# Kernel tuning notes

Measured on AMD Instinct MI355X. Metric: run time of the kernel, lower is better.

The kernel has to match this reference:

```python
import jax, jax.numpy as jnp
import numpy as np

HIDDEN = 2048
INTER = 768
N_EXPERTS = 16
TOP_K = 2
B, S = 4, 2048


def setup_inputs() -> dict:
    key = jax.random.key(0)
    ks = jax.random.split(key, 5)
    scale = 0.02
    return {
        "hidden_states": jax.random.normal(ks[0], (B, S, HIDDEN), dtype=jnp.float32),
        # nn.Linear weight layout: [out_features, in_features]
        "gate_w": jax.random.normal(ks[1], (N_EXPERTS, HIDDEN), dtype=jnp.float32) * scale,
        "w_gate": jax.random.normal(ks[2], (N_EXPERTS, INTER, HIDDEN), dtype=jnp.float32) * scale,
        "w_up": jax.random.normal(ks[3], (N_EXPERTS, INTER, HIDDEN), dtype=jnp.float32) * scale,
        "w_down": jax.random.normal(ks[4], (N_EXPERTS, HIDDEN, INTER), dtype=jnp.float32) * scale,
    }


def _moe_forward(hidden_states, gate_w, w_gate, w_up, w_down):
    b, s, h = hidden_states.shape
    x = hidden_states.reshape(-1, h)                      # [T, H]
    t = x.shape[0]
    logits = x @ gate_w.T                                 # [T, E]
    probs = jax.nn.softmax(logits, axis=-1)
    top_vals, top_idx = jax.lax.top_k(probs, TOP_K)       # [T, K]
    top_vals = top_vals / jnp.sum(top_vals, axis=-1, keepdims=True)
    # combine weights per token per expert (zero if not routed)
    comb = jnp.zeros((t, N_EXPERTS), dtype=x.dtype)
    comb = comb.at[jnp.arange(t)[:, None], top_idx].add(top_vals)  # [T, E]

    out = jnp.zeros_like(x)
    for e in range(N_EXPERTS):  # small fixed loop over experts
        g = x @ w_gate[e].T                               # [T, I]
        u = x @ w_up[e].T                                 # [T, I]
        y = (jax.nn.silu(g) * u) @ w_down[e].T            # [T, H]
        out = out + comb[:, e:e + 1] * y
    return out.reshape(b, s, h)


def reference(hidden_states, gate_w, w_gate, w_up, w_down):
    return _moe_forward(hidden_states, gate_w, w_gate, w_up, w_down)
```

## Files before the change

### kernel.cpp

```cpp
#include <hip/hip_runtime.h>
#include <hip/hip_bf16.h>

#define NTOK 8192
#define HID 2048
#define INTER 768
#define NEXP 16

typedef __bf16 bf16x8 __attribute__((ext_vector_type(8)));
typedef float f32x4 __attribute__((ext_vector_type(4)));

typedef const __attribute__((address_space(1))) void gvoid_t;
typedef __attribute__((address_space(3))) void lvoid_t;

static __device__ __forceinline__ void load_lds16(const void* g, void* l) {
  __builtin_amdgcn_global_load_lds((gvoid_t*)g, (lvoid_t*)l, 16, 0, 0);
}

static __device__ __forceinline__ unsigned short f2bf(float f) {
  unsigned int u = __float_as_uint(f);
  u += 0x7FFFu + ((u >> 16) & 1u);
  return (unsigned short)(u >> 16);
}

static __device__ __forceinline__ float bf2f(unsigned short b) {
  return __uint_as_float(((unsigned int)b) << 16);
}

#define SYNC_PIPE                                     \
  asm volatile("s_waitcnt vmcnt(0)" ::: "memory");    \
  __builtin_amdgcn_s_barrier();

__global__ __launch_bounds__(256) void cvt3_kernel(
    const float* __restrict__ s0, const float* __restrict__ s1, const float* __restrict__ s2,
    unsigned short* __restrict__ dst0, unsigned short* __restrict__ dst1,
    unsigned short* __restrict__ dst2, int n) {
  const float* src = (blockIdx.y == 0) ? s0 : (blockIdx.y == 1) ? s1 : s2;
  unsigned short* dst = (blockIdx.y == 0) ? dst0 : (blockIdx.y == 1) ? dst1 : dst2;
  int i = (blockIdx.x * 256 + threadIdx.x) * 4;
  int stride = gridDim.x * 256 * 4;
  for (; i < n; i += stride) {
    float4 v = *reinterpret_cast<const float4*>(src + i);
    ushort4 o;
    o.x = f2bf(v.x); o.y = f2bf(v.y); o.z = f2bf(v.z); o.w = f2bf(v.w);
    *reinterpret_cast<ushort4*>(dst + i) = o;
  }
}

__global__ __launch_bounds__(256) void router_kernel(const float* __restrict__ x,
                                                     const float* __restrict__ gw,
                                                     int* __restrict__ te,
                                                     float* __restrict__ tw,
                                                     unsigned short* __restrict__ Xb) {
  const int lane = threadIdx.x & 63;
  const int wid = threadIdx.x >> 6;
  const int t0 = (blockIdx.x * 4 + wid) * 2;
  const float4* xa = reinterpret_cast<const float4*>(x + (size_t)t0 * HID);
  const float4* xb = xa + HID / 4;
  const float4* g4 = reinterpret_cast<const float4*>(gw);

  float4 va[8], vb[8];
#pragma unroll
  for (int j = 0; j < 8; ++j) {
    va[j] = xa[lane + 64 * j];
    vb[j] = xb[lane + 64 * j];
  }
  ushort4* oa = reinterpret_cast<ushort4*>(Xb + (size_t)t0 * HID);
  ushort4* ob = oa + HID / 4;
#pragma unroll
  for (int j = 0; j < 8; ++j) {
    ushort4 u;
    u.x = f2bf(va[j].x); u.y = f2bf(va[j].y); u.z = f2bf(va[j].z); u.w = f2bf(va[j].w);
    oa[lane + 64 * j] = u;
    u.x = f2bf(vb[j].x); u.y = f2bf(vb[j].y); u.z = f2bf(vb[j].z); u.w = f2bf(vb[j].w);
    ob[lane + 64 * j] = u;
  }

  float accA[NEXP], accB[NEXP];
#pragma unroll
  for (int e = 0; e < NEXP; ++e) { accA[e] = 0.f; accB[e] = 0.f; }
#pragma unroll
  for (int e = 0; e < NEXP; ++e) {
#pragma unroll
    for (int j = 0; j < 8; ++j) {
      float4 g = g4[e * (HID / 4) + lane + 64 * j];
      accA[e] += va[j].x * g.x + va[j].y * g.y + va[j].z * g.z + va[j].w * g.w;
      accB[e] += vb[j].x * g.x + vb[j].y * g.y + vb[j].z * g.z + vb[j].w * g.w;
    }
  }
#pragma unroll
  for (int e = 0; e < NEXP; ++e) {
#pragma unroll
    for (int m = 32; m >= 1; m >>= 1) {
      accA[e] += __shfl_xor(accA[e], m);
      accB[e] += __shfl_xor(accB[e], m);
    }
  }
  if (lane == 0) {
#pragma unroll
    for (int k = 0; k < 2; ++k) {
      const float* acc = k ? accB : accA;
      int t = t0 + k;
      float b0 = -1e30f; int i0 = 0;
#pragma unroll
      for (int e = 0; e < NEXP; ++e) { if (acc[e] > b0) { b0 = acc[e]; i0 = e; } }
      float b1 = -1e30f; int i1 = 0;
#pragma unroll
      for (int e = 0; e < NEXP; ++e) { if (e != i0 && acc[e] > b1) { b1 = acc[e]; i1 = e; } }
      float w0 = 1.f / (1.f + __expf(b1 - b0));
      te[2 * t] = i0; te[2 * t + 1] = i1;
      tw[2 * t] = w0; tw[2 * t + 1] = 1.f - w0;
    }
  }
}

__global__ __launch_bounds__(256) void build_kernel(
    const int* __restrict__ te, const float* __restrict__ tw,
    int* __restrict__ counts, int* __restrict__ offsets,
    int* __restrict__ tok_flat, float* __restrict__ w_flat,
    int* __restrict__ tok_slot,
    int* __restrict__ tile_map, int* __restrict__ n_tiles) {
  __shared__ int lds_cnt[NEXP][257];
  __shared__ int lds_off[NEXP];
  const int tid = threadIdx.x;
  const int lane = tid & 63;
  const int wv = tid >> 6;

  int cnt[NEXP];
#pragma unroll
  for (int ex = 0; ex < NEXP; ++ex) cnt[ex] = 0;
  for (int i = 0; i < 64; ++i) {
    int e = te[tid * 64 + i];
#pragma unroll
    for (int ex = 0; ex < NEXP; ++ex) cnt[ex] += (e == ex) ? 1 : 0;
  }
#pragma unroll
  for (int ex = 0; ex < NEXP; ++ex) lds_cnt[ex][tid] = cnt[ex];
  __syncthreads();

  for (int ex = wv * 4; ex < wv * 4 + 4; ++ex) {
    int carry = 0;
    for (int c = 0; c < 4; ++c) {
      int v = lds_cnt[ex][c * 64 + lane];
      int s = v;
#pragma unroll
      for (int d = 1; d < 64; d <<= 1) {
        int o = __shfl_up(s, d);
        if (lane >= d) s += o;
      }
      lds_cnt[ex][c * 64 + lane] = carry + s - v;
      carry += __shfl(s, 63);
    }
    if (lane == 0) lds_cnt[ex][256] = carry;
  }
  __syncthreads();

  if (tid == 0) {
    int run = 0, nt = 0;
    for (int e = 0; e < NEXP; ++e) {
      int tot = lds_cnt[e][256];
      counts[e] = tot;
      offsets[e] = run;
      lds_off[e] = run;
      for (int m0 = 0; m0 < tot; m0 += 128) tile_map[nt++] = (e << 16) | m0;
      run += tot;
    }
    *n_tiles = nt;
  }
  __syncthreads();

  int base[NEXP];
#pragma unroll
  for (int ex = 0; ex < NEXP; ++ex) base[ex] = lds_off[ex] + lds_cnt[ex][tid];
  for (int i = 0; i < 64; ++i) {
    int idx = tid * 64 + i;
    int e = te[idx];
    float w = tw[idx];
    int pos = 0;
#pragma unroll
    for (int ex = 0; ex < NEXP; ++ex) {
      if (e == ex) { pos = base[ex]; base[ex] = pos + 1; }
    }
    tok_flat[pos] = idx >> 1;
    w_flat[pos] = w;
    tok_slot[idx] = pos;
  }
}

__global__ __launch_bounds__(256, 2) void gemm_gu_kernel(
    const unsigned short* __restrict__ Xb,
    const unsigned short* __restrict__ Wg,
    const unsigned short* __restrict__ Wu,
    const int* __restrict__ counts, const int* __restrict__ offsets,
    const int* __restrict__ tok_flat,
    const int* __restrict__ tile_map, const int* __restrict__ n_tiles,
    unsigned short* __restrict__ Hf) {
  const int bid = blockIdx.x;
  const int cpx = gridDim.x >> 3;
  const int wg = (bid & 7) * cpx + (bid >> 3);
  const int y = wg / 6;
  if (y >= *n_tiles) return;
  const int xb = wg - y * 6;
  const int tm = tile_map[y];
  const int e = tm >> 16, m0 = tm & 0xFFFF;
  const int cnt = counts[e];
  const int off = offsets[e];
  const int n0 = xb * 128;

  __shared__ __align__(16) unsigned short As0[128 * 32], As1[128 * 32];
  __shared__ __align__(16) unsigned short Bg0[128 * 32], Bg1[128 * 32];
  __shared__ __align__(16) unsigned short Bu0[128 * 32], Bu1[128 * 32];

  const int tid = threadIdx.x;
  const int lane = tid & 63;
  const int wid = tid >> 6;
  const int rl = tid >> 2;
  const int srcc = ((tid & 3) ^ ((tid >> 3) & 3)) * 8;
  const int d0 = tid * 8;
  const int d1 = d0 + 64 * 32;

  const int r0 = m0 + rl, r1 = r0 + 64;
  const int s0 = (r0 < cnt) ? off + r0 : off;
  const int s1 = (r1 < cnt) ? off + r1 : off;
  const unsigned short* aptr0 = Xb + (size_t)tok_flat[s0] * HID + srcc;
  const unsigned short* aptr1 = Xb + (size_t)tok_flat[s1] * HID + srcc;
  const unsigned short* gptr0 = Wg + ((size_t)e * INTER + n0 + rl) * HID + srcc;
  const unsigned short* gptr1 = gptr0 + (size_t)64 * HID;
  const unsigned short* uptr0 = Wu + ((size_t)e * INTER + n0 + rl) * HID + srcc;
  const unsigned short* uptr1 = uptr0 + (size_t)64 * HID;

  f32x4 zero = {0.f, 0.f, 0.f, 0.f};
  f32x4 accG[4][4], accU[4][4];
#pragma unroll
  for (int i = 0; i < 4; ++i)
#pragma unroll
    for (int j = 0; j < 4; ++j) { accG[i][j] = zero; accU[i][j] = zero; }

  const int wm = (wid >> 1) * 64;
  const int wn = (wid & 1) * 64;
  const int fr = lane & 15;
  const int cs = (((lane >> 4) ^ ((lane >> 1) & 3)) * 8);

#define STAGE_GU(AS, BGS, BUS, kt)           \
  {                                          \
    load_lds16(aptr0 + (kt), (AS) + d0);     \
    load_lds16(aptr1 + (kt), (AS) + d1);     \
    load_lds16(gptr0 + (kt), (BGS) + d0);    \
    load_lds16(gptr1 + (kt), (BGS) + d1);    \
    load_lds16(uptr0 + (kt), (BUS) + d0);    \
    load_lds16(uptr1 + (kt), (BUS) + d1);    \
  }

#define COMPUTE_GU(AS, BGS, BUS)                                                       \
  {                                                                                    \
    bf16x8 af[4], bg[4], bu[4];                                                        \
    _Pragma("unroll") for (int i = 0; i < 4; ++i) {                                    \
      af[i] = *reinterpret_cast<const bf16x8*>((AS) + (wm + i * 16 + fr) * 32 + cs);   \
      bg[i] = *reinterpret_cast<const bf16x8*>((BGS) + (wn + i * 16 + fr) * 32 + cs);  \
      bu[i] = *reinterpret_cast<const bf16x8*>((BUS) + (wn + i * 16 + fr) * 32 + cs);  \
    }                                                                                  \
    _Pragma("unroll") for (int i = 0; i < 4; ++i)                                      \
      _Pragma("unroll") for (int j = 0; j < 4; ++j) {                                  \
        accG[i][j] = __builtin_amdgcn_mfma_f32_16x16x32_bf16(af[i], bg[j], accG[i][j], 0, 0, 0); \
        accU[i][j] = __builtin_amdgcn_mfma_f32_16x16x32_bf16(af[i], bu[j], accU[i][j], 0, 0, 0); \
      }                                                                                \
  }

  STAGE_GU(As0, Bg0, Bu0, 0);
  SYNC_PIPE
#pragma unroll 1
  for (int kt = 0; kt < HID; kt += 64) {
    STAGE_GU(As1, Bg1, Bu1, kt + 32);
    COMPUTE_GU(As0, Bg0, Bu0);
    SYNC_PIPE
    if (kt + 64 < HID) STAGE_GU(As0, Bg0, Bu0, kt + 64);
    COMPUTE_GU(As1, Bg1, Bu1);
    SYNC_PIPE
  }
#undef STAGE_GU
#undef COMPUTE_GU

  const int lr = (lane >> 4) * 4;
  const int lc = lane & 15;
#pragma unroll
  for (int i = 0; i < 4; ++i) {
#pragma unroll
    for (int r = 0; r < 4; ++r) {
      int m = wm + i * 16 + lr + r;
      if (m0 + m < cnt) {
        size_t base = (size_t)(off + m0 + m) * INTER + (size_t)(n0 + wn + lc);
#pragma unroll
        for (int j = 0; j < 4; ++j) {
          float g = accG[i][j][r];
          float u = accU[i][j][r];
          float h = g / (1.f + __expf(-g)) * u;
          Hf[base + j * 16] = f2bf(h);
        }
      }
    }
  }
}

__global__ __launch_bounds__(256, 3) void gemm_y_kernel(
    const unsigned short* __restrict__ Hf,
    const unsigned short* __restrict__ Wd,
    const int* __restrict__ counts, const int* __restrict__ offsets,
    const float* __restrict__ w_flat,
    const int* __restrict__ tile_map, const int* __restrict__ n_tiles,
    unsigned short* __restrict__ Yf) {
  const int bid = blockIdx.x;
  const int cpx = gridDim.x >> 3;
  const int wg = (bid & 7) * cpx + (bid >> 3);
  const int y = wg / 16;
  if (y >= *n_tiles) return;
  const int xb = wg - y * 16;
  const int tm = tile_map[y];
  const int e = tm >> 16, m0 = tm & 0xFFFF;
  const int cnt = counts[e];
  const int off = offsets[e];
  const int n0 = xb * 128;

  __shared__ __align__(16) unsigned short As0[128 * 32], As1[128 * 32];
  __shared__ __align__(16) unsigned short Bs0[128 * 32], Bs1[128 * 32];

  const int tid = threadIdx.x;
  const int lane = tid & 63;
  const int wid = tid >> 6;
  const int rl = tid >> 2;
  const int srcc = ((tid & 3) ^ ((tid >> 3) & 3)) * 8;
  const int d0 = tid * 8;
  const int d1 = d0 + 64 * 32;

  const int r0 = m0 + rl, r1 = r0 + 64;
  const int s0 = (r0 < cnt) ? off + r0 : off;
  const int s1 = (r1 < cnt) ? off + r1 : off;
  const unsigned short* aptr0 = Hf + (size_t)s0 * INTER + srcc;
  const unsigned short* aptr1 = Hf + (size_t)s1 * INTER + srcc;
  const unsigned short* bptr0 = Wd + ((size_t)e * HID + n0 + rl) * INTER + srcc;
  const unsigned short* bptr1 = bptr0 + (size_t)64 * INTER;

  f32x4 zero = {0.f, 0.f, 0.f, 0.f};
  f32x4 acc[4][4];
#pragma unroll
  for (int i = 0; i < 4; ++i)
#pragma unroll
    for (int j = 0; j < 4; ++j) acc[i][j] = zero;

  const int wm = (wid >> 1) * 64;
  const int wn = (wid & 1) * 64;
  const int fr = lane & 15;
  const int cs = (((lane >> 4) ^ ((lane >> 1) & 3)) * 8);

#define STAGE_Y(AS, BS, kt)               \
  {                                       \
    load_lds16(aptr0 + (kt), (AS) + d0);  \
    load_lds16(aptr1 + (kt), (AS) + d1);  \
    load_lds16(bptr0 + (kt), (BS) + d0);  \
    load_lds16(bptr1 + (kt), (BS) + d1);  \
  }

#define COMPUTE_Y(AS, BS)                                                              \
  {                                                                                    \
    bf16x8 af[4], bf_[4];                                                              \
    _Pragma("unroll") for (int i = 0; i < 4; ++i) {                                    \
      af[i] = *reinterpret_cast<const bf16x8*>((AS) + (wm + i * 16 + fr) * 32 + cs);   \
      bf_[i] = *reinterpret_cast<const bf16x8*>((BS) + (wn + i * 16 + fr) * 32 + cs);  \
    }                                                                                  \
    _Pragma("unroll") for (int i = 0; i < 4; ++i)                                      \
      _Pragma("unroll") for (int j = 0; j < 4; ++j)                                    \
        acc[i][j] = __builtin_amdgcn_mfma_f32_16x16x32_bf16(af[i], bf_[j], acc[i][j], 0, 0, 0); \
  }

  STAGE_Y(As0, Bs0, 0);
  SYNC_PIPE
#pragma unroll 1
  for (int kt = 0; kt < INTER; kt += 64) {
    STAGE_Y(As1, Bs1, kt + 32);
    COMPUTE_Y(As0, Bs0);
    SYNC_PIPE
    if (kt + 64 < INTER) STAGE_Y(As0, Bs0, kt + 64);
    COMPUTE_Y(As1, Bs1);
    SYNC_PIPE
  }
#undef STAGE_Y
#undef COMPUTE_Y

  const int lr = (lane >> 4) * 4;
  const int lc = lane & 15;
#pragma unroll
  for (int i = 0; i < 4; ++i) {
#pragma unroll
    for (int r = 0; r < 4; ++r) {
      int m = wm + i * 16 + lr + r;
      if (m0 + m < cnt) {
        int slot = off + m0 + m;
        float w = w_flat[slot];
        size_t base = (size_t)slot * HID + (size_t)(n0 + wn + lc);
#pragma unroll
        for (int j = 0; j < 4; ++j) Yf[base + j * 16] = f2bf(w * acc[i][j][r]);
      }
    }
  }
}

__global__ __launch_bounds__(256) void combine_kernel(const unsigned short* __restrict__ Yf,
                                                      const int* __restrict__ tok_slot,
                                                      float* __restrict__ out) {
  const int t = blockIdx.x;
  const int c = threadIdx.x * 8;
  const int s0 = tok_slot[2 * t];
  const int s1 = tok_slot[2 * t + 1];
  const ushort4* p0 = reinterpret_cast<const ushort4*>(Yf + (size_t)s0 * HID + c);
  const ushort4* p1 = reinterpret_cast<const ushort4*>(Yf + (size_t)s1 * HID + c);
  ushort4 a0 = p0[0], a1 = p0[1];
  ushort4 b0 = p1[0], b1 = p1[1];
  float4 o0, o1;
  o0.x = bf2f(a0.x) + bf2f(b0.x);
  o0.y = bf2f(a0.y) + bf2f(b0.y);
  o0.z = bf2f(a0.z) + bf2f(b0.z);
  o0.w = bf2f(a0.w) + bf2f(b0.w);
  o1.x = bf2f(a1.x) + bf2f(b1.x);
  o1.y = bf2f(a1.y) + bf2f(b1.y);
  o1.z = bf2f(a1.z) + bf2f(b1.z);
  o1.w = bf2f(a1.w) + bf2f(b1.w);
  float4* op = reinterpret_cast<float4*>(out + (size_t)t * HID + c);
  op[0] = o0;
  op[1] = o1;
}

extern "C" void kernel_launch(void* const* d_in, const int* in_sizes, int n_in,
                              void* d_out, int out_size, void* d_ws, size_t ws_size,
                              hipStream_t stream) {
  const float* x  = (const float*)d_in[0];
  const float* gw = (const float*)d_in[1];
  const float* wg = (const float*)d_in[2];
  const float* wu = (const float*)d_in[3];
  const float* wd = (const float*)d_in[4];
  float* out = (float*)d_out;
  char* ws = (char*)d_ws;

  int*   counts   = (int*)(ws + 0);
  int*   offsets  = (int*)(ws + 128);
  int*   n_tiles  = (int*)(ws + 192);
  int*   tile_map = (int*)(ws + 256);
  int*   te       = (int*)(ws + 1024);
  float* tw       = (float*)(ws + 66560);
  int*   tok_flat = (int*)(ws + 132096);
  float* w_flat   = (float*)(ws + 197632);
  unsigned short* Xb  = (unsigned short*)(ws + 263168);
  unsigned short* Wgb = (unsigned short*)(ws + 33817600);
  unsigned short* Wub = (unsigned short*)(ws + 84149248);
  unsigned short* Wdb = (unsigned short*)(ws + 134480896);
  unsigned short* Hf  = (unsigned short*)(ws + 184812544);
  int*   tok_slot = (int*)(ws + 209978368);
  unsigned short* Yf  = Wgb;

  cvt3_kernel<<<dim3(1024, 3), 256, 0, stream>>>(wg, wu, wd, Wgb, Wub, Wdb,
                                                 NEXP * INTER * HID);

  router_kernel<<<NTOK / 8, 256, 0, stream>>>(x, gw, te, tw, Xb);
  build_kernel<<<1, 256, 0, stream>>>(te, tw, counts, offsets, tok_flat, w_flat,
                                      tok_slot, tile_map, n_tiles);

  gemm_gu_kernel<<<144 * 6, 256, 0, stream>>>(
      Xb, Wgb, Wub, counts, offsets, tok_flat, tile_map, n_tiles, Hf);
  gemm_y_kernel<<<144 * 16, 256, 0, stream>>>(
      Hf, Wdb, counts, offsets, w_flat, tile_map, n_tiles, Yf);
  combine_kernel<<<NTOK, 256, 0, stream>>>(Yf, tok_slot, out);
}
```

Measured before the change: 453.9 us.

## Halve GEMM N-tile to 64, raise occupancy, fuse weight cast with router

Both expert GEMMs now use a 128x64 output tile instead of 128x128, which doubles the grid and cuts per-block LDS and accumulator registers so launch bounds can ask for more resident blocks. The weight bf16 conversion and the router now run as one launch, with the router blocks in an extra grid row. Smaller tiles mean more A-tile reloads and lower arithmetic intensity per block. The fused launch drops one kernel launch and lets the router overlap with the conversion.

After: 550.3 us. 1.21x slower.

```diff
diff --git a/kernel.cpp b/kernel.cpp
--- a/kernel.cpp
+++ b/kernel.cpp
@@ -30,27 +30,25 @@
   asm volatile("s_waitcnt vmcnt(0)" ::: "memory");    \
   __builtin_amdgcn_s_barrier();
 
-__global__ __launch_bounds__(256) void cvt3_kernel(
-    const float* __restrict__ s0, const float* __restrict__ s1, const float* __restrict__ s2,
-    unsigned short* __restrict__ dst0, unsigned short* __restrict__ dst1,
-    unsigned short* __restrict__ dst2, int n) {
-  const float* src = (blockIdx.y == 0) ? s0 : (blockIdx.y == 1) ? s1 : s2;
-  unsigned short* dst = (blockIdx.y == 0) ? dst0 : (blockIdx.y == 1) ? dst1 : dst2;
-  int i = (blockIdx.x * 256 + threadIdx.x) * 4;
-  int stride = gridDim.x * 256 * 4;
-  for (; i < n; i += stride) {
-    float4 v = *reinterpret_cast<const float4*>(src + i);
-    ushort4 o;
-    o.x = f2bf(v.x); o.y = f2bf(v.y); o.z = f2bf(v.z); o.w = f2bf(v.w);
-    *reinterpret_cast<ushort4*>(dst + i) = o;
-  }
-}
-
-__global__ __launch_bounds__(256) void router_kernel(const float* __restrict__ x,
-                                                     const float* __restrict__ gw,
-                                                     int* __restrict__ te,
-                                                     float* __restrict__ tw,
-                                                     unsigned short* __restrict__ Xb) {
+__global__ __launch_bounds__(256) void prologue_kernel(
+    const float* __restrict__ wg, const float* __restrict__ wu, const float* __restrict__ wd,
+    unsigned short* __restrict__ Wgb, unsigned short* __restrict__ Wub,
+    unsigned short* __restrict__ Wdb, int n,
+    const float* __restrict__ x, const float* __restrict__ gw,
+    int* __restrict__ te, float* __restrict__ tw, unsigned short* __restrict__ Xb) {
+  if (blockIdx.y < 3) {
+    const float* src = (blockIdx.y == 0) ? wg : (blockIdx.y == 1) ? wu : wd;
+    unsigned short* dst = (blockIdx.y == 0) ? Wgb : (blockIdx.y == 1) ? Wub : Wdb;
+    int i = (blockIdx.x * 256 + threadIdx.x) * 4;
+    int stride = gridDim.x * 256 * 4;
+    for (; i < n; i += stride) {
+      float4 v = *reinterpret_cast<const float4*>(src + i);
+      ushort4 o;
+      o.x = f2bf(v.x); o.y = f2bf(v.y); o.z = f2bf(v.z); o.w = f2bf(v.w);
+      *reinterpret_cast<ushort4*>(dst + i) = o;
+    }
+    return;
+  }
   const int lane = threadIdx.x & 63;
   const int wid = threadIdx.x >> 6;
   const int t0 = (blockIdx.x * 4 + wid) * 2;
@@ -186,7 +184,7 @@
   }
 }
 
-__global__ __launch_bounds__(256, 2) void gemm_gu_kernel(
+__global__ __launch_bounds__(256, 3) void gemm_gu_kernel(
     const unsigned short* __restrict__ Xb,
     const unsigned short* __restrict__ Wg,
     const unsigned short* __restrict__ Wu,
@@ -197,18 +195,18 @@
   const int bid = blockIdx.x;
   const int cpx = gridDim.x >> 3;
   const int wg = (bid & 7) * cpx + (bid >> 3);
-  const int y = wg / 6;
+  const int y = wg / 12;
   if (y >= *n_tiles) return;
-  const int xb = wg - y * 6;
+  const int xb = wg - y * 12;
   const int tm = tile_map[y];
   const int e = tm >> 16, m0 = tm & 0xFFFF;
   const int cnt = counts[e];
   const int off = offsets[e];
-  const int n0 = xb * 128;
+  const int n0 = xb * 64;
 
   __shared__ __align__(16) unsigned short As0[128 * 32], As1[128 * 32];
-  __shared__ __align__(16) unsigned short Bg0[128 * 32], Bg1[128 * 32];
-  __shared__ __align__(16) unsigned short Bu0[128 * 32], Bu1[128 * 32];
+  __shared__ __align__(16) unsigned short Bg0[64 * 32], Bg1[64 * 32];
+  __shared__ __align__(16) unsigned short Bu0[64 * 32], Bu1[64 * 32];
 
   const int tid = threadIdx.x;
   const int lane = tid & 63;
@@ -224,19 +222,17 @@
   const unsigned short* aptr0 = Xb + (size_t)tok_flat[s0] * HID + srcc;
   const unsigned short* aptr1 = Xb + (size_t)tok_flat[s1] * HID + srcc;
   const unsigned short* gptr0 = Wg + ((size_t)e * INTER + n0 + rl) * HID + srcc;
-  const unsigned short* gptr1 = gptr0 + (size_t)64 * HID;
   const unsigned short* uptr0 = Wu + ((size_t)e * INTER + n0 + rl) * HID + srcc;
-  const unsigned short* uptr1 = uptr0 + (size_t)64 * HID;
 
   f32x4 zero = {0.f, 0.f, 0.f, 0.f};
-  f32x4 accG[4][4], accU[4][4];
+  f32x4 accG[4][2], accU[4][2];
 #pragma unroll
   for (int i = 0; i < 4; ++i)
 #pragma unroll
-    for (int j = 0; j < 4; ++j) { accG[i][j] = zero; accU[i][j] = zero; }
+    for (int j = 0; j < 2; ++j) { accG[i][j] = zero; accU[i][j] = zero; }
 
   const int wm = (wid >> 1) * 64;
-  const int wn = (wid & 1) * 64;
+  const int wn = (wid & 1) * 32;
   const int fr = lane & 15;
   const int cs = (((lane >> 4) ^ ((lane >> 1) & 3)) * 8);
 
@@ -245,21 +241,20 @@
     load_lds16(aptr0 + (kt), (AS) + d0);     \
     load_lds16(aptr1 + (kt), (AS) + d1);     \
     load_lds16(gptr0 + (kt), (BGS) + d0);    \
-    load_lds16(gptr1 + (kt), (BGS) + d1);    \
     load_lds16(uptr0 + (kt), (BUS) + d0);    \
-    load_lds16(uptr1 + (kt), (BUS) + d1);    \
   }
 
 #define COMPUTE_GU(AS, BGS, BUS)                                                       \
   {                                                                                    \
-    bf16x8 af[4], bg[4], bu[4];                                                        \
-    _Pragma("unroll") for (int i = 0; i < 4; ++i) {                                    \
+    bf16x8 af[4], bg[2], bu[2];                                                        \
+    _Pragma("unroll") for (int i = 0; i < 4; ++i)                                      \
       af[i] = *reinterpret_cast<const bf16x8*>((AS) + (wm + i * 16 + fr) * 32 + cs);   \
-      bg[i] = *reinterpret_cast<const bf16x8*>((BGS) + (wn + i * 16 + fr) * 32 + cs);  \
-      bu[i] = *reinterpret_cast<const bf16x8*>((BUS) + (wn + i * 16 + fr) * 32 + cs);  \
+    _Pragma("unroll") for (int j = 0; j < 2; ++j) {                                    \
+      bg[j] = *reinterpret_cast<const bf16x8*>((BGS) + (wn + j * 16 + fr) * 32 + cs);  \
+      bu[j] = *reinterpret_cast<const bf16x8*>((BUS) + (wn + j * 16 + fr) * 32 + cs);  \
     }                                                                                  \
     _Pragma("unroll") for (int i = 0; i < 4; ++i)                                      \
-      _Pragma("unroll") for (int j = 0; j < 4; ++j) {                                  \
+      _Pragma("unroll") for (int j = 0; j < 2; ++j) {                                  \
         accG[i][j] = __builtin_amdgcn_mfma_f32_16x16x32_bf16(af[i], bg[j], accG[i][j], 0, 0, 0); \
         accU[i][j] = __builtin_amdgcn_mfma_f32_16x16x32_bf16(af[i], bu[j], accU[i][j], 0, 0, 0); \
       }                                                                                \
@@ -289,7 +284,7 @@
       if (m0 + m < cnt) {
         size_t base = (size_t)(off + m0 + m) * INTER + (size_t)(n0 + wn + lc);
 #pragma unroll
-        for (int j = 0; j < 4; ++j) {
+        for (int j = 0; j < 2; ++j) {
           float g = accG[i][j][r];
           float u = accU[i][j][r];
           float h = g / (1.f + __expf(-g)) * u;
@@ -300,7 +295,7 @@
   }
 }
 
-__global__ __launch_bounds__(256, 3) void gemm_y_kernel(
+__global__ __launch_bounds__(256, 4) void gemm_y_kernel(
     const unsigned short* __restrict__ Hf,
     const unsigned short* __restrict__ Wd,
     const int* __restrict__ counts, const int* __restrict__ offsets,
@@ -310,17 +305,17 @@
   const int bid = blockIdx.x;
   const int cpx = gridDim.x >> 3;
   const int wg = (bid & 7) * cpx + (bid >> 3);
-  const int y = wg / 16;
+  const int y = wg / 32;
   if (y >= *n_tiles) return;
-  const int xb = wg - y * 16;
+  const int xb = wg - y * 32;
   const int tm = tile_map[y];
   const int e = tm >> 16, m0 = tm & 0xFFFF;
   const int cnt = counts[e];
   const int off = offsets[e];
-  const int n0 = xb * 128;
+  const int n0 = xb * 64;
 
   __shared__ __align__(16) unsigned short As0[128 * 32], As1[128 * 32];
-  __shared__ __align__(16) unsigned short Bs0[128 * 32], Bs1[128 * 32];
+  __shared__ __align__(16) unsigned short Bs0[64 * 32], Bs1[64 * 32];
 
   const int tid = threadIdx.x;
   const int lane = tid & 63;
@@ -336,17 +331,16 @@
   const unsigned short* aptr0 = Hf + (size_t)s0 * INTER + srcc;
   const unsigned short* aptr1 = Hf + (size_t)s1 * INTER + srcc;
   const unsigned short* bptr0 = Wd + ((size_t)e * HID + n0 + rl) * INTER + srcc;
-  const unsigned short* bptr1 = bptr0 + (size_t)64 * INTER;
 
   f32x4 zero = {0.f, 0.f, 0.f, 0.f};
-  f32x4 acc[4][4];
+  f32x4 acc[4][2];
 #pragma unroll
   for (int i = 0; i < 4; ++i)
 #pragma unroll
-    for (int j = 0; j < 4; ++j) acc[i][j] = zero;
+    for (int j = 0; j < 2; ++j) acc[i][j] = zero;
 
   const int wm = (wid >> 1) * 64;
-  const int wn = (wid & 1) * 64;
+  const int wn = (wid & 1) * 32;
   const int fr = lane & 15;
   const int cs = (((lane >> 4) ^ ((lane >> 1) & 3)) * 8);
 
@@ -355,18 +349,17 @@
     load_lds16(aptr0 + (kt), (AS) + d0);  \
     load_lds16(aptr1 + (kt), (AS) + d1);  \
     load_lds16(bptr0 + (kt), (BS) + d0);  \
-    load_lds16(bptr1 + (kt), (BS) + d1);  \
   }
 
 #define COMPUTE_Y(AS, BS)                                                              \
   {                                                                                    \
-    bf16x8 af[4], bf_[4];                                                              \
-    _Pragma("unroll") for (int i = 0; i < 4; ++i) {                                    \
+    bf16x8 af[4], bf_[2];                                                              \
+    _Pragma("unroll") for (int i = 0; i < 4; ++i)                                      \
       af[i] = *reinterpret_cast<const bf16x8*>((AS) + (wm + i * 16 + fr) * 32 + cs);   \
-      bf_[i] = *reinterpret_cast<const bf16x8*>((BS) + (wn + i * 16 + fr) * 32 + cs);  \
-    }                                                                                  \
+    _Pragma("unroll") for (int j = 0; j < 2; ++j)                                      \
+      bf_[j] = *reinterpret_cast<const bf16x8*>((BS) + (wn + j * 16 + fr) * 32 + cs);  \
     _Pragma("unroll") for (int i = 0; i < 4; ++i)                                      \
-      _Pragma("unroll") for (int j = 0; j < 4; ++j)                                    \
+      _Pragma("unroll") for (int j = 0; j < 2; ++j)                                    \
         acc[i][j] = __builtin_amdgcn_mfma_f32_16x16x32_bf16(af[i], bf_[j], acc[i][j], 0, 0, 0); \
   }
 
@@ -396,7 +389,7 @@
         float w = w_flat[slot];
         size_t base = (size_t)slot * HID + (size_t)(n0 + wn + lc);
 #pragma unroll
-        for (int j = 0; j < 4; ++j) Yf[base + j * 16] = f2bf(w * acc[i][j][r]);
+        for (int j = 0; j < 2; ++j) Yf[base + j * 16] = f2bf(w * acc[i][j][r]);
       }
     }
   }
@@ -454,16 +447,14 @@
   int*   tok_slot = (int*)(ws + 209978368);
   unsigned short* Yf  = Wgb;
 
-  cvt3_kernel<<<dim3(1024, 3), 256, 0, stream>>>(wg, wu, wd, Wgb, Wub, Wdb,
-                                                 NEXP * INTER * HID);
-
-  router_kernel<<<NTOK / 8, 256, 0, stream>>>(x, gw, te, tw, Xb);
+  prologue_kernel<<<dim3(1024, 4), 256, 0, stream>>>(
+      wg, wu, wd, Wgb, Wub, Wdb, NEXP * INTER * HID, x, gw, te, tw, Xb);
   build_kernel<<<1, 256, 0, stream>>>(te, tw, counts, offsets, tok_flat, w_flat,
                                       tok_slot, tile_map, n_tiles);
 
-  gemm_gu_kernel<<<144 * 6, 256, 0, stream>>>(
+  gemm_gu_kernel<<<144 * 12, 256, 0, stream>>>(
       Xb, Wgb, Wub, counts, offsets, tok_flat, tile_map, n_tiles, Hf);
-  gemm_y_kernel<<<144 * 16, 256, 0, stream>>>(
+  gemm_y_kernel<<<144 * 32, 256, 0, stream>>>(
       Hf, Wdb, counts, offsets, w_flat, tile_map, n_tiles, Yf);
   combine_kernel<<<NTOK, 256, 0, stream>>>(Yf, tok_slot, out);
 }
```

## Load expert weight fragments directly into registers, bypassing LDS staging

Applied to the files above, without the earlier changes.

In both grouped GEMM kernels, the B operand (expert weights) is now read from global memory straight into per-wave MFMA register fragments instead of being staged through double-buffered LDS. Only the gathered token tile A stays in LDS. A sched_barrier is added after each sync so the compiler cannot move instructions across it. This cuts LDS traffic and shared-memory footprint and may raise occupancy. In exchange, the two waves sharing a column block each load the same weights, and the global loads are 16-byte row-strided reads that are less coalesced and may stall MFMA issue.

New measurement: 638.2 us. 40.6% more time.

```diff
diff --git a/kernel.cpp b/kernel.cpp
--- a/kernel.cpp
+++ b/kernel.cpp
@@ -28,7 +28,8 @@
 
 #define SYNC_PIPE                                     \
   asm volatile("s_waitcnt vmcnt(0)" ::: "memory");    \
-  __builtin_amdgcn_s_barrier();
+  __builtin_amdgcn_s_barrier();                       \
+  __builtin_amdgcn_sched_barrier(0);
 
 __global__ __launch_bounds__(256) void cvt3_kernel(
     const float* __restrict__ s0, const float* __restrict__ s1, const float* __restrict__ s2,
@@ -207,76 +208,83 @@
   const int n0 = xb * 128;
 
   __shared__ __align__(16) unsigned short As0[128 * 32], As1[128 * 32];
-  __shared__ __align__(16) unsigned short Bg0[128 * 32], Bg1[128 * 32];
-  __shared__ __align__(16) unsigned short Bu0[128 * 32], Bu1[128 * 32];
 
   const int tid = threadIdx.x;
   const int lane = tid & 63;
   const int wid = tid >> 6;
-  const int rl = tid >> 2;
   const int srcc = ((tid & 3) ^ ((tid >> 3) & 3)) * 8;
   const int d0 = tid * 8;
   const int d1 = d0 + 64 * 32;
 
+  const int rl = tid >> 2;
   const int r0 = m0 + rl, r1 = r0 + 64;
   const int s0 = (r0 < cnt) ? off + r0 : off;
   const int s1 = (r1 < cnt) ? off + r1 : off;
   const unsigned short* aptr0 = Xb + (size_t)tok_flat[s0] * HID + srcc;
   const unsigned short* aptr1 = Xb + (size_t)tok_flat[s1] * HID + srcc;
-  const unsigned short* gptr0 = Wg + ((size_t)e * INTER + n0 + rl) * HID + srcc;
-  const unsigned short* gptr1 = gptr0 + (size_t)64 * HID;
-  const unsigned short* uptr0 = Wu + ((size_t)e * INTER + n0 + rl) * HID + srcc;
-  const unsigned short* uptr1 = uptr0 + (size_t)64 * HID;
-
-  f32x4 zero = {0.f, 0.f, 0.f, 0.f};
-  f32x4 accG[4][4], accU[4][4];
-#pragma unroll
-  for (int i = 0; i < 4; ++i)
-#pragma unroll
-    for (int j = 0; j < 4; ++j) { accG[i][j] = zero; accU[i][j] = zero; }
 
   const int wm = (wid >> 1) * 64;
   const int wn = (wid & 1) * 64;
   const int fr = lane & 15;
+  const int fc = (lane >> 4) * 8;
   const int cs = (((lane >> 4) ^ ((lane >> 1) & 3)) * 8);
 
-#define STAGE_GU(AS, BGS, BUS, kt)           \
-  {                                          \
-    load_lds16(aptr0 + (kt), (AS) + d0);     \
-    load_lds16(aptr1 + (kt), (AS) + d1);     \
-    load_lds16(gptr0 + (kt), (BGS) + d0);    \
-    load_lds16(gptr1 + (kt), (BGS) + d1);    \
-    load_lds16(uptr0 + (kt), (BUS) + d0);    \
-    load_lds16(uptr1 + (kt), (BUS) + d1);    \
-  }
-
-#define COMPUTE_GU(AS, BGS, BUS)                                                       \
+  const unsigned short* bgp = Wg + ((size_t)e * INTER + n0 + wn + fr) * HID + fc;
+  const unsigned short* bup = Wu + ((size_t)e * INTER + n0 + wn + fr) * HID + fc;
+
+  f32x4 zero = {0.f, 0.f, 0.f, 0.f};
+  f32x4 accG[4][4], accU[4][4];
+#pragma unroll
+  for (int i = 0; i < 4; ++i)
+#pragma unroll
+    for (int j = 0; j < 4; ++j) { accG[i][j] = zero; accU[i][j] = zero; }
+
+  bf16x8 bgA[4], buA[4], bgB[4], buB[4];
+
+#define STAGE_A(AS, kt)                     \
+  {                                         \
+    load_lds16(aptr0 + (kt), (AS) + d0);    \
+    load_lds16(aptr1 + (kt), (AS) + d1);    \
+  }
+
+#define LOADB(BG, BU, kt)                                                              \
   {                                                                                    \
-    bf16x8 af[4], bg[4], bu[4];                                                        \
-    _Pragma("unroll") for (int i = 0; i < 4; ++i) {                                    \
+    _Pragma("unroll") for (int j = 0; j < 4; ++j) {                                    \
+      BG[j] = *reinterpret_cast<const bf16x8*>(bgp + (size_t)j * 16 * HID + (kt));     \
+      BU[j] = *reinterpret_cast<const bf16x8*>(bup + (size_t)j * 16 * HID + (kt));     \
+    }                                                                                  \
+  }
+
+#define COMPUTE_GU(AS, BG, BU)                                                         \
+  {                                                                                    \
+    bf16x8 af[4];                                                                      \
+    _Pragma("unroll") for (int i = 0; i < 4; ++i)                                      \
       af[i] = *reinterpret_cast<const bf16x8*>((AS) + (wm + i * 16 + fr) * 32 + cs);   \
-      bg[i] = *reinterpret_cast<const bf16x8*>((BGS) + (wn + i * 16 + fr) * 32 + cs);  \
-      bu[i] = *reinterpret_cast<const bf16x8*>((BUS) + (wn + i * 16 + fr) * 32 + cs);  \
-    }                                                                                  \
     _Pragma("unroll") for (int i = 0; i < 4; ++i)                                      \
       _Pragma("unroll") for (int j = 0; j < 4; ++j) {                                  \
-        accG[i][j] = __builtin_amdgcn_mfma_f32_16x16x32_bf16(af[i], bg[j], accG[i][j], 0, 0, 0); \
-        accU[i][j] = __builtin_amdgcn_mfma_f32_16x16x32_bf16(af[i], bu[j], accU[i][j], 0, 0, 0); \
+        accG[i][j] = __builtin_amdgcn_mfma_f32_16x16x32_bf16(af[i], BG[j], accG[i][j], 0, 0, 0); \
+        accU[i][j] = __builtin_amdgcn_mfma_f32_16x16x32_bf16(af[i], BU[j], accU[i][j], 0, 0, 0); \
       }                                                                                \
   }
 
-  STAGE_GU(As0, Bg0, Bu0, 0);
+  STAGE_A(As0, 0);
+  LOADB(bgA, buA, 0);
   SYNC_PIPE
 #pragma unroll 1
   for (int kt = 0; kt < HID; kt += 64) {
-    STAGE_GU(As1, Bg1, Bu1, kt + 32);
-    COMPUTE_GU(As0, Bg0, Bu0);
+    STAGE_A(As1, kt + 32);
+    LOADB(bgB, buB, kt + 32);
+    COMPUTE_GU(As0, bgA, buA);
     SYNC_PIPE
-    if (kt + 64 < HID) STAGE_GU(As0, Bg0, Bu0, kt + 64);
-    COMPUTE_GU(As1, Bg1, Bu1);
+    if (kt + 64 < HID) {
+      STAGE_A(As0, kt + 64);
+      LOADB(bgA, buA, kt + 64);
+    }
+    COMPUTE_GU(As1, bgB, buB);
     SYNC_PIPE
   }
-#undef STAGE_GU
+#undef STAGE_A
+#undef LOADB
 #undef COMPUTE_GU
 
   const int lr = (lane >> 4) * 4;
@@ -320,68 +328,78 @@
   const int n0 = xb * 128;
 
   __shared__ __align__(16) unsigned short As0[128 * 32], As1[128 * 32];
-  __shared__ __align__(16) unsigned short Bs0[128 * 32], Bs1[128 * 32];
 
   const int tid = threadIdx.x;
   const int lane = tid & 63;
   const int wid = tid >> 6;
-  const int rl = tid >> 2;
   const int srcc = ((tid & 3) ^ ((tid >> 3) & 3)) * 8;
   const int d0 = tid * 8;
   const int d1 = d0 + 64 * 32;
 
+  const int rl = tid >> 2;
   const int r0 = m0 + rl, r1 = r0 + 64;
   const int s0 = (r0 < cnt) ? off + r0 : off;
   const int s1 = (r1 < cnt) ? off + r1 : off;
   const unsigned short* aptr0 = Hf + (size_t)s0 * INTER + srcc;
   const unsigned short* aptr1 = Hf + (size_t)s1 * INTER + srcc;
-  const unsigned short* bptr0 = Wd + ((size_t)e * HID + n0 + rl) * INTER + srcc;
-  const unsigned short* bptr1 = bptr0 + (size_t)64 * INTER;
-
-  f32x4 zero = {0.f, 0.f, 0.f, 0.f};
-  f32x4 acc[4][4];
-#pragma unroll
-  for (int i = 0; i < 4; ++i)
-#pragma unroll
-    for (int j = 0; j < 4; ++j) acc[i][j] = zero;
 
   const int wm = (wid >> 1) * 64;
   const int wn = (wid & 1) * 64;
   const int fr = lane & 15;
+  const int fc = (lane >> 4) * 8;
   const int cs = (((lane >> 4) ^ ((lane >> 1) & 3)) * 8);
 
-#define STAGE_Y(AS, BS, kt)               \
-  {                                       \
-    load_lds16(aptr0 + (kt), (AS) + d0);  \
-    load_lds16(aptr1 + (kt), (AS) + d1);  \
-    load_lds16(bptr0 + (kt), (BS) + d0);  \
-    load_lds16(bptr1 + (kt), (BS) + d1);  \
-  }
-
-#define COMPUTE_Y(AS, BS)                                                              \
+  const unsigned short* bp = Wd + ((size_t)e * HID + n0 + wn + fr) * INTER + fc;
+
+  f32x4 zero = {0.f, 0.f, 0.f, 0.f};
+  f32x4 acc[4][4];
+#pragma unroll
+  for (int i = 0; i < 4; ++i)
+#pragma unroll
+    for (int j = 0; j < 4; ++j) acc[i][j] = zero;
+
+  bf16x8 bA[4], bB[4];
+
+#define STAGE_A(AS, kt)                     \
+  {                                         \
+    load_lds16(aptr0 + (kt), (AS) + d0);    \
+    load_lds16(aptr1 + (kt), (AS) + d1);    \
+  }
+
+#define LOADB(BV, kt)                                                                  \
   {                                                                                    \
-    bf16x8 af[4], bf_[4];                                                              \
-    _Pragma("unroll") for (int i = 0; i < 4; ++i) {                                    \
+    _Pragma("unroll") for (int j = 0; j < 4; ++j)                                      \
+      BV[j] = *reinterpret_cast<const bf16x8*>(bp + (size_t)j * 16 * INTER + (kt));    \
+  }
+
+#define COMPUTE_Y(AS, BV)                                                              \
+  {                                                                                    \
+    bf16x8 af[4];                                                                      \
+    _Pragma("unroll") for (int i = 0; i < 4; ++i)                                      \
       af[i] = *reinterpret_cast<const bf16x8*>((AS) + (wm + i * 16 + fr) * 32 + cs);   \
-      bf_[i] = *reinterpret_cast<const bf16x8*>((BS) + (wn + i * 16 + fr) * 32 + cs);  \
-    }                                                                                  \
     _Pragma("unroll") for (int i = 0; i < 4; ++i)                                      \
       _Pragma("unroll") for (int j = 0; j < 4; ++j)                                    \
-        acc[i][j] = __builtin_amdgcn_mfma_f32_16x16x32_bf16(af[i], bf_[j], acc[i][j], 0, 0, 0); \
-  }
-
-  STAGE_Y(As0, Bs0, 0);
+        acc[i][j] = __builtin_amdgcn_mfma_f32_16x16x32_bf16(af[i], BV[j], acc[i][j], 0, 0, 0); \
+  }
+
+  STAGE_A(As0, 0);
+  LOADB(bA, 0);
   SYNC_PIPE
 #pragma unroll 1
   for (int kt = 0; kt < INTER; kt += 64) {
-    STAGE_Y(As1, Bs1, kt + 32);
-    COMPUTE_Y(As0, Bs0);
+    STAGE_A(As1, kt + 32);
+    LOADB(bB, kt + 32);
+    COMPUTE_Y(As0, bA);
     SYNC_PIPE
-    if (kt + 64 < INTER) STAGE_Y(As0, Bs0, kt + 64);
-    COMPUTE_Y(As1, Bs1);
+    if (kt + 64 < INTER) {
+      STAGE_A(As0, kt + 64);
+      LOADB(bA, kt + 64);
+    }
+    COMPUTE_Y(As1, bB);
     SYNC_PIPE
   }
-#undef STAGE_Y
+#undef STAGE_A
+#undef LOADB
 #undef COMPUTE_Y
 
   const int lr = (lane >> 4) * 4;
@@ -456,7 +474,6 @@
 
   cvt3_kernel<<<dim3(1024, 3), 256, 0, stream>>>(wg, wu, wd, Wgb, Wub, Wdb,
                                                  NEXP * INTER * HID);
-
   router_kernel<<<NTOK / 8, 256, 0, stream>>>(x, gw, te, tw, Xb);
   build_kernel<<<1, 256, 0, stream>>>(te, tw, counts, offsets, tok_flat, w_flat,
                                       tok_slot, tile_map, n_tiles);
```
